# Kernel tuning notes

Measured on AMD Instinct MI355X. Metric: run time of the kernel, lower is better.

Reference implementation:

```python
import jax, jax.numpy as jnp
import numpy as np

B, C, H, W = 8, 256, 48, 48
CR = C // 8  # query/key channel dim of the 1x1 conv projections


def setup_inputs() -> dict:
    key = jax.random.key(0)
    ks = jax.random.split(key, 8)
    s = 0.05  # weight scale
    return {
        "feat_map": jax.random.normal(ks[0], (B, C, H, W), dtype=jnp.float32),
        "w1": jax.random.normal(ks[1], (CR, C), dtype=jnp.float32) * s,
        "b1": jax.random.normal(ks[2], (CR,), dtype=jnp.float32) * s,
        "w2": jax.random.normal(ks[3], (CR, C), dtype=jnp.float32) * s,
        "b2": jax.random.normal(ks[4], (CR,), dtype=jnp.float32) * s,
        "w3": jax.random.normal(ks[5], (C, C), dtype=jnp.float32) * s,
        "b3": jax.random.normal(ks[6], (C,), dtype=jnp.float32) * s,
        "gamma": jnp.asarray(0.1, dtype=jnp.float32),  # torch inits to 0; nonzero for a meaningful baseline
    }


def reference(feat_map, w1, b1, w2, b2, w3, b3, gamma):
    b, c, h, w = feat_map.shape
    n = h * w
    x = feat_map.reshape(b, c, n)                     # [B,C,N]
    # 1x1 convs == per-pixel channel matmuls
    q = jnp.einsum('dc,bcn->bnd', w1, x) + b1         # [B,N,C/8]
    k = jnp.einsum('dc,bcn->bdn', w2, x) + b2[None, :, None]  # [B,C/8,N]
    attn = jax.nn.softmax(jnp.einsum('bnd,bdm->bnm', q, k), axis=-1)  # [B,N,N]
    v = jnp.einsum('dc,bcn->bdn', w3, x) + b3[None, :, None]  # [B,C,N]
    # out[b,c,i] = sum_j v[b,c,j] * attn[b,i,j]  (matches bmm(v, attn^T))
    refine = jnp.einsum('bcj,bij->bci', v, attn).reshape(b, c, h, w)
    return gamma * refine + feat_map
```

## Files before the change

kernel.cpp:

```cpp
#include <hip/hip_runtime.h>
#include <stdint.h>

#define NB  8
#define NC  256
#define NCR 32
#define NSP 2304
#define LOG2E 1.44269504088896340736f

typedef __attribute__((ext_vector_type(8))) short short8;
typedef __attribute__((ext_vector_type(4))) float f32x4;
typedef __attribute__((ext_vector_type(4))) unsigned short us4;
typedef __attribute__((ext_vector_type(2))) unsigned int u32x2;

__device__ __forceinline__ unsigned short f2bf(float f) {
  union { float f; unsigned u; } a; a.f = f;
  unsigned r = (a.u + 0x7FFFu + ((a.u >> 16) & 1u)) >> 16;
  return (unsigned short)r;
}

__device__ __forceinline__ float fexp2(float x) {
#if __has_builtin(__builtin_amdgcn_exp2f)
  return __builtin_amdgcn_exp2f(x);
#else
  return __exp2f(x);
#endif
}

__device__ __forceinline__ u32x2 pack4bf(float a, float b, float c, float d) {
  u32x2 r;
#if __has_builtin(__builtin_amdgcn_cvt_pk_bf16_f32)
  typedef __attribute__((ext_vector_type(2))) __bf16 bf2;
  union { bf2 v; unsigned u; } lo, hi;
  lo.v = __builtin_amdgcn_cvt_pk_bf16_f32(a, b);
  hi.v = __builtin_amdgcn_cvt_pk_bf16_f32(c, d);
  r[0] = lo.u; r[1] = hi.u;
#else
  r[0] = (unsigned)f2bf(a) | ((unsigned)f2bf(b) << 16);
  r[1] = (unsigned)f2bf(c) | ((unsigned)f2bf(d) << 16);
#endif
  return r;
}

typedef __attribute__((address_space(1))) const void* gvoidp;
typedef __attribute__((address_space(3))) void* lvoidp;
#define GLOADLDS16(g, l) __builtin_amdgcn_global_load_lds((gvoidp)(g), (lvoidp)(l), 16, 0, 0)

__global__ __launch_bounds__(256) void k_proj(const float* __restrict__ x,
    const float* __restrict__ w1, const float* __restrict__ b1,
    const float* __restrict__ w2, const float* __restrict__ b2,
    const float* __restrict__ w3, const float* __restrict__ b3,
    unsigned short* __restrict__ Q, unsigned short* __restrict__ K,
    unsigned short* __restrict__ V) {
  __shared__ unsigned short xs[32][264];
  const int n0 = blockIdx.x * 32, b = blockIdx.y;
  const int t = threadIdx.x, lane = t & 63, wave = t >> 6;
  const int col = lane & 15, quad = lane >> 4;
  const float* xb = x + (size_t)b * NC * NSP;
#pragma unroll
  for (int p = 0; p < 8; ++p) {
    const int crow = (t >> 3) + p * 32;
    const int n4 = (t & 7) * 4;
    float4 v = *(const float4*)(xb + (size_t)crow * NSP + n0 + n4);
    xs[n4 + 0][crow] = f2bf(v.x);
    xs[n4 + 1][crow] = f2bf(v.y);
    xs[n4 + 2][crow] = f2bf(v.z);
    xs[n4 + 3][crow] = f2bf(v.w);
  }
  __syncthreads();
  const f32x4 zero4 = {0.f, 0.f, 0.f, 0.f};
  f32x4 acc[5][2];
#pragma unroll
  for (int i = 0; i < 5; ++i)
#pragma unroll
    for (int j = 0; j < 2; ++j) acc[i][j] = zero4;

  for (int kc = 0; kc < 8; ++kc) {
    short8 bf[2];
#pragma unroll
    for (int nt = 0; nt < 2; ++nt)
      bf[nt] = *(const short8*)&xs[nt * 16 + col][kc * 32 + quad * 8];
#pragma unroll
    for (int ml = 0; ml < 5; ++ml) {
      const int m0 = (wave * 5 + ml) * 16;
      const float* wbase; int roff;
      if (m0 < 32)      { wbase = w1; roff = m0; }
      else if (m0 < 64) { wbase = w2; roff = m0 - 32; }
      else              { wbase = w3; roff = m0 - 64; }
      const float* wp = wbase + (size_t)(roff + col) * NC + kc * 32 + quad * 8;
      float4 f0 = *(const float4*)wp;
      float4 f1 = *(const float4*)(wp + 4);
      short8 af;
      af[0] = f2bf(f0.x); af[1] = f2bf(f0.y); af[2] = f2bf(f0.z); af[3] = f2bf(f0.w);
      af[4] = f2bf(f1.x); af[5] = f2bf(f1.y); af[6] = f2bf(f1.z); af[7] = f2bf(f1.w);
#pragma unroll
      for (int nt = 0; nt < 2; ++nt)
        acc[ml][nt] = __builtin_amdgcn_mfma_f32_16x16x32_bf16(af, bf[nt], acc[ml][nt], 0, 0, 0);
    }
  }
#pragma unroll
  for (int ml = 0; ml < 5; ++ml) {
    const int m0 = (wave * 5 + ml) * 16;
    const float* bias;
    if (m0 < 32)      bias = b1 + m0;
    else if (m0 < 64) bias = b2 + (m0 - 32);
    else              bias = b3 + (m0 - 64);
    float bv[4];
#pragma unroll
    for (int r = 0; r < 4; ++r) bv[r] = bias[quad * 4 + r];
    if (m0 < 64) {
      unsigned short* dst = (m0 < 32) ? Q : K;
      const float scl = (m0 < 32) ? LOG2E : 1.0f;
      const int d0 = (m0 & 31) + quad * 4;
#pragma unroll
      for (int nt = 0; nt < 2; ++nt) {
        const int n = n0 + nt * 16 + col;
        us4 pk;
#pragma unroll
        for (int r = 0; r < 4; ++r) pk[r] = f2bf((acc[ml][nt][r] + bv[r]) * scl);
        *(us4*)(dst + ((size_t)b * NSP + n) * NCR + d0) = pk;
      }
    } else {
      const int cbase = m0 - 64 + quad * 4;
#pragma unroll
      for (int nt = 0; nt < 2; ++nt) {
        const int n = n0 + nt * 16 + col;
#pragma unroll
        for (int r = 0; r < 4; ++r)
          V[((size_t)b * NC + cbase + r) * NSP + n] = f2bf(acc[ml][nt][r] + bv[r]);
      }
    }
  }
}

__global__ __launch_bounds__(192) void k_attn(const unsigned short* __restrict__ Q,
    const unsigned short* __restrict__ K, const unsigned short* __restrict__ V,
    const float* __restrict__ feat, const float* __restrict__ gamma,
    float* __restrict__ out) {
  __shared__ __align__(16) unsigned short smem[23296];
  unsigned short* Vs = smem;
  unsigned short* Ps = smem + 16384;
  const int i0 = blockIdx.x * 48, ch = blockIdx.y * 128, b = blockIdx.z;
  const int t = threadIdx.x, lane = t & 63, wave = t >> 6;
  const int col = lane & 15, quad = lane >> 4;
  const int iw = i0 + wave * 16;
  const unsigned short* Qb = Q + (size_t)b * NSP * NCR;
  const unsigned short* Kb = K + (size_t)b * NSP * NCR;
  const unsigned short* Vb = V + (size_t)b * NC * NSP;
  unsigned short* PsW = Ps + wave * 2304;

  const short8 qa = *(const short8*)(Qb + (size_t)(iw + col) * NCR + quad * 8);
  const f32x4 zero4 = {0.f, 0.f, 0.f, 0.f};
  f32x4 acc[8];
#pragma unroll
  for (int ct = 0; ct < 8; ++ct) acc[ct] = zero4;
  float rs = 0.f;
  const int r8 = lane >> 3, pc = lane & 7, jcs = pc ^ r8;

  short8 kb[4];
#pragma unroll
  for (int mt = 0; mt < 4; ++mt)
    kb[mt] = *(const short8*)(Kb + (size_t)(mt * 16 + col) * NCR + quad * 8);
#pragma unroll
  for (int cix = 0; cix < 6; ++cix) {
    const int q = wave * 6 + cix;
    if (q < 16) {
      const unsigned short* g = Vb + (size_t)(ch + q * 8 + r8) * NSP + jcs * 8;
      GLOADLDS16(g, Vs + q * 512);
    }
  }
#pragma unroll
  for (int mt = 0; mt < 4; ++mt) {
    f32x4 s = __builtin_amdgcn_mfma_f32_16x16x32_bf16(kb[mt], qa, zero4, 0, 0, 0);
    const float e0 = fexp2(s[0]), e1 = fexp2(s[1]), e2 = fexp2(s[2]), e3 = fexp2(s[3]);
    rs += (e0 + e1) + (e2 + e3);
    *(u32x2*)(PsW + col * 72 + mt * 16 + quad * 4) = pack4bf(e0, e1, e2, e3);
  }

  for (int kc = 0; kc < 36; ++kc) {
    __syncthreads();
    const int bufc = kc & 1, bufn = bufc ^ 1;
    const int j1 = (kc + 1) * 64;
    const bool more = (kc + 1 < 36);
    if (more) {
#pragma unroll
      for (int mt = 0; mt < 4; ++mt)
        kb[mt] = *(const short8*)(Kb + (size_t)(j1 + mt * 16 + col) * NCR + quad * 8);
#pragma unroll
      for (int cix = 0; cix < 6; ++cix) {
        const int q = wave * 6 + cix;
        if (q < 16) {
          const unsigned short* g = Vb + (size_t)(ch + q * 8 + r8) * NSP + j1 + jcs * 8;
          GLOADLDS16(g, Vs + bufn * 8192 + q * 512);
        }
      }
    }
    const unsigned short* pwc = PsW + bufc * 1152;
    const unsigned short* vsc = Vs + bufc * 8192;
#pragma unroll
    for (int kk = 0; kk < 2; ++kk) {
      const short8 pa = *(const short8*)(pwc + col * 72 + kk * 32 + quad * 8);
#pragma unroll
      for (int ct = 0; ct < 8; ++ct) {
        const short8 vbf = *(const short8*)(vsc + (ct * 16 + col) * 64 +
                                            (((kk * 4 + quad) ^ (col & 7)) * 8));
        acc[ct] = __builtin_amdgcn_mfma_f32_16x16x32_bf16(pa, vbf, acc[ct], 0, 0, 0);
      }
    }
    if (more) {
      unsigned short* pwn = PsW + bufn * 1152;
#pragma unroll
      for (int mt = 0; mt < 4; ++mt) {
        f32x4 s = __builtin_amdgcn_mfma_f32_16x16x32_bf16(kb[mt], qa, zero4, 0, 0, 0);
        const float e0 = fexp2(s[0]), e1 = fexp2(s[1]), e2 = fexp2(s[2]), e3 = fexp2(s[3]);
        rs += (e0 + e1) + (e2 + e3);
        *(u32x2*)(pwn + col * 72 + mt * 16 + quad * 4) = pack4bf(e0, e1, e2, e3);
      }
    }
  }

  rs += __shfl_xor(rs, 16, 64);
  rs += __shfl_xor(rs, 32, 64);
  const float g = gamma[0];
  float rinv[4];
#pragma unroll
  for (int r = 0; r < 4; ++r) rinv[r] = g / __shfl(rs, quad * 4 + r, 64);

  const float* fb = feat + (size_t)b * NC * NSP;
  float* ob = out + (size_t)b * NC * NSP;
#pragma unroll
  for (int ct = 0; ct < 8; ++ct) {
    const size_t a0 = (size_t)(ch + ct * 16 + col) * NSP + iw + quad * 4;
    float4 f = *(const float4*)(fb + a0);
    float4 o;
    o.x = acc[ct][0] * rinv[0] + f.x;
    o.y = acc[ct][1] * rinv[1] + f.y;
    o.z = acc[ct][2] * rinv[2] + f.z;
    o.w = acc[ct][3] * rinv[3] + f.w;
    *(float4*)(ob + a0) = o;
  }
}

#define OFF_Q  0UL
#define OFF_K  1179648UL
#define OFF_V  2359296UL

extern "C" void kernel_launch(void* const* d_in, const int* in_sizes, int n_in,
                              void* d_out, int out_size, void* d_ws, size_t ws_size,
                              hipStream_t stream) {
  const float* feat  = (const float*)d_in[0];
  const float* w1    = (const float*)d_in[1];
  const float* b1    = (const float*)d_in[2];
  const float* w2    = (const float*)d_in[3];
  const float* b2    = (const float*)d_in[4];
  const float* w3    = (const float*)d_in[5];
  const float* b3    = (const float*)d_in[6];
  const float* gamma = (const float*)d_in[7];
  float* out = (float*)d_out;
  char* ws = (char*)d_ws;
  unsigned short* Q = (unsigned short*)(ws + OFF_Q);
  unsigned short* K = (unsigned short*)(ws + OFF_K);
  unsigned short* V = (unsigned short*)(ws + OFF_V);

  hipLaunchKernelGGL(k_proj, dim3(72, NB), dim3(256), 0, stream,
                     feat, w1, b1, w2, b2, w3, b3, Q, K, V);
  hipLaunchKernelGGL(k_attn, dim3(48, 2, NB), dim3(192), 0, stream,
                     Q, K, V, feat, gamma, out);
}
```

Before: 167.7 us.

## Split attention key dimension in two halves and combine partials in separate kernel

The attention kernel now splits the key/value sequence into two halves across blockIdx.y, doubling the grid from 768 to 1536 blocks. Each block uses 32-wide key chunks and a smaller LDS footprint, then writes unnormalized fp32 partial outputs and row sums to workspace. A new combine kernel adds the two partials, normalizes by the summed row sums, applies gamma and adds the residual. This trades extra global traffic and a third launch (about 37MB written and read back) for more parallelism and occupancy. It also drops the running softmax max, relying on scores staying small as the original did.

```diff
diff --git a/kernel.cpp b/kernel.cpp
--- a/kernel.cpp
+++ b/kernel.cpp
@@ -134,19 +134,20 @@
 
 __global__ __launch_bounds__(192) void k_attn(const unsigned short* __restrict__ Q,
     const unsigned short* __restrict__ K, const unsigned short* __restrict__ V,
-    const float* __restrict__ feat, const float* __restrict__ gamma,
-    float* __restrict__ out) {
-  __shared__ __align__(16) unsigned short smem[23296];
+    float* __restrict__ Op, float* __restrict__ lp) {
+  __shared__ __align__(16) unsigned short smem[12032];
   unsigned short* Vs = smem;
-  unsigned short* Ps = smem + 16384;
-  const int i0 = blockIdx.x * 48, ch = blockIdx.y * 128, b = blockIdx.z;
+  unsigned short* Ps = smem + 8192;
+  const int i0 = blockIdx.x * 48, b = blockIdx.z;
+  const int ch = (blockIdx.y & 1) * 128, jh = blockIdx.y >> 1;
+  const int jb = jh * 1152;
   const int t = threadIdx.x, lane = t & 63, wave = t >> 6;
   const int col = lane & 15, quad = lane >> 4;
   const int iw = i0 + wave * 16;
   const unsigned short* Qb = Q + (size_t)b * NSP * NCR;
   const unsigned short* Kb = K + (size_t)b * NSP * NCR;
   const unsigned short* Vb = V + (size_t)b * NC * NSP;
-  unsigned short* PsW = Ps + wave * 2304;
+  unsigned short* PsW = Ps + wave * 1280;
 
   const short8 qa = *(const short8*)(Qb + (size_t)(iw + col) * NCR + quad * 8);
   const f32x4 zero4 = {0.f, 0.f, 0.f, 0.f};
@@ -154,95 +155,106 @@
 #pragma unroll
   for (int ct = 0; ct < 8; ++ct) acc[ct] = zero4;
   float rs = 0.f;
-  const int r8 = lane >> 3, pc = lane & 7, jcs = pc ^ r8;
-
-  short8 kb[4];
-#pragma unroll
-  for (int mt = 0; mt < 4; ++mt)
-    kb[mt] = *(const short8*)(Kb + (size_t)(mt * 16 + col) * NCR + quad * 8);
-#pragma unroll
-  for (int cix = 0; cix < 6; ++cix) {
-    const int q = wave * 6 + cix;
-    if (q < 16) {
-      const unsigned short* g = Vb + (size_t)(ch + q * 8 + r8) * NSP + jcs * 8;
+  const int r4 = lane >> 2, pc = lane & 3, jcs = pc ^ (r4 & 3);
+
+  short8 kb[2];
+#pragma unroll
+  for (int mt = 0; mt < 2; ++mt)
+    kb[mt] = *(const short8*)(Kb + (size_t)(jb + mt * 16 + col) * NCR + quad * 8);
+#pragma unroll
+  for (int cix = 0; cix < 3; ++cix) {
+    const int q = wave * 3 + cix;
+    if (q < 8) {
+      const unsigned short* g = Vb + (size_t)(ch + q * 16 + r4) * NSP + jb + jcs * 8;
       GLOADLDS16(g, Vs + q * 512);
     }
   }
 #pragma unroll
-  for (int mt = 0; mt < 4; ++mt) {
+  for (int mt = 0; mt < 2; ++mt) {
     f32x4 s = __builtin_amdgcn_mfma_f32_16x16x32_bf16(kb[mt], qa, zero4, 0, 0, 0);
     const float e0 = fexp2(s[0]), e1 = fexp2(s[1]), e2 = fexp2(s[2]), e3 = fexp2(s[3]);
     rs += (e0 + e1) + (e2 + e3);
-    *(u32x2*)(PsW + col * 72 + mt * 16 + quad * 4) = pack4bf(e0, e1, e2, e3);
+    *(u32x2*)(PsW + col * 40 + mt * 16 + quad * 4) = pack4bf(e0, e1, e2, e3);
   }
 
   for (int kc = 0; kc < 36; ++kc) {
     __syncthreads();
     const int bufc = kc & 1, bufn = bufc ^ 1;
-    const int j1 = (kc + 1) * 64;
+    const int j1 = jb + (kc + 1) * 32;
     const bool more = (kc + 1 < 36);
     if (more) {
 #pragma unroll
-      for (int mt = 0; mt < 4; ++mt)
+      for (int mt = 0; mt < 2; ++mt)
         kb[mt] = *(const short8*)(Kb + (size_t)(j1 + mt * 16 + col) * NCR + quad * 8);
 #pragma unroll
-      for (int cix = 0; cix < 6; ++cix) {
-        const int q = wave * 6 + cix;
-        if (q < 16) {
-          const unsigned short* g = Vb + (size_t)(ch + q * 8 + r8) * NSP + j1 + jcs * 8;
-          GLOADLDS16(g, Vs + bufn * 8192 + q * 512);
+      for (int cix = 0; cix < 3; ++cix) {
+        const int q = wave * 3 + cix;
+        if (q < 8) {
+          const unsigned short* g = Vb + (size_t)(ch + q * 16 + r4) * NSP + j1 + jcs * 8;
+          GLOADLDS16(g, Vs + bufn * 4096 + q * 512);
         }
       }
     }
-    const unsigned short* pwc = PsW + bufc * 1152;
-    const unsigned short* vsc = Vs + bufc * 8192;
-#pragma unroll
-    for (int kk = 0; kk < 2; ++kk) {
-      const short8 pa = *(const short8*)(pwc + col * 72 + kk * 32 + quad * 8);
-#pragma unroll
-      for (int ct = 0; ct < 8; ++ct) {
-        const short8 vbf = *(const short8*)(vsc + (ct * 16 + col) * 64 +
-                                            (((kk * 4 + quad) ^ (col & 7)) * 8));
-        acc[ct] = __builtin_amdgcn_mfma_f32_16x16x32_bf16(pa, vbf, acc[ct], 0, 0, 0);
-      }
+    const unsigned short* pwc = PsW + bufc * 640;
+    const unsigned short* vsc = Vs + bufc * 4096;
+    const short8 pa = *(const short8*)(pwc + col * 40 + quad * 8);
+#pragma unroll
+    for (int ct = 0; ct < 8; ++ct) {
+      const short8 vbf = *(const short8*)(vsc + (ct * 16 + col) * 32 +
+                                          ((quad ^ (col & 3)) * 8));
+      acc[ct] = __builtin_amdgcn_mfma_f32_16x16x32_bf16(pa, vbf, acc[ct], 0, 0, 0);
     }
     if (more) {
-      unsigned short* pwn = PsW + bufn * 1152;
-#pragma unroll
-      for (int mt = 0; mt < 4; ++mt) {
+      unsigned short* pwn = PsW + bufn * 640;
+#pragma unroll
+      for (int mt = 0; mt < 2; ++mt) {
         f32x4 s = __builtin_amdgcn_mfma_f32_16x16x32_bf16(kb[mt], qa, zero4, 0, 0, 0);
         const float e0 = fexp2(s[0]), e1 = fexp2(s[1]), e2 = fexp2(s[2]), e3 = fexp2(s[3]);
         rs += (e0 + e1) + (e2 + e3);
-        *(u32x2*)(pwn + col * 72 + mt * 16 + quad * 4) = pack4bf(e0, e1, e2, e3);
+        *(u32x2*)(pwn + col * 40 + mt * 16 + quad * 4) = pack4bf(e0, e1, e2, e3);
       }
     }
   }
 
   rs += __shfl_xor(rs, 16, 64);
   rs += __shfl_xor(rs, 32, 64);
+  if (((blockIdx.y & 1) == 0) && quad == 0)
+    lp[((size_t)jh * NB + b) * NSP + iw + col] = rs;
+
+  float* Ob = Op + (((size_t)jh * NB + b) * NC + ch) * NSP;
+#pragma unroll
+  for (int ct = 0; ct < 8; ++ct)
+    *(f32x4*)(Ob + (size_t)(ct * 16 + col) * NSP + iw + quad * 4) = acc[ct];
+}
+
+__global__ __launch_bounds__(256) void k_combine(const float* __restrict__ Op,
+    const float* __restrict__ lp, const float* __restrict__ feat,
+    const float* __restrict__ gamma, float* __restrict__ out) {
+  const int tid = blockIdx.x * 256 + threadIdx.x;
+  const int b = tid / (NC * NSP / 4);
+  const int rem = tid - b * (NC * NSP / 4);
+  const int c = rem / (NSP / 4);
+  const int i4 = (rem - c * (NSP / 4)) * 4;
+  const size_t a = ((size_t)b * NC + c) * NSP + i4;
+  const float4 o0 = *(const float4*)(Op + a);
+  const float4 o1 = *(const float4*)(Op + (size_t)NB * NC * NSP + a);
+  const float4 l0 = *(const float4*)(lp + (size_t)b * NSP + i4);
+  const float4 l1 = *(const float4*)(lp + (size_t)(NB + b) * NSP + i4);
+  const float4 ft = *(const float4*)(feat + a);
   const float g = gamma[0];
-  float rinv[4];
-#pragma unroll
-  for (int r = 0; r < 4; ++r) rinv[r] = g / __shfl(rs, quad * 4 + r, 64);
-
-  const float* fb = feat + (size_t)b * NC * NSP;
-  float* ob = out + (size_t)b * NC * NSP;
-#pragma unroll
-  for (int ct = 0; ct < 8; ++ct) {
-    const size_t a0 = (size_t)(ch + ct * 16 + col) * NSP + iw + quad * 4;
-    float4 f = *(const float4*)(fb + a0);
-    float4 o;
-    o.x = acc[ct][0] * rinv[0] + f.x;
-    o.y = acc[ct][1] * rinv[1] + f.y;
-    o.z = acc[ct][2] * rinv[2] + f.z;
-    o.w = acc[ct][3] * rinv[3] + f.w;
-    *(float4*)(ob + a0) = o;
-  }
+  float4 o;
+  o.x = (o0.x + o1.x) * (g / (l0.x + l1.x)) + ft.x;
+  o.y = (o0.y + o1.y) * (g / (l0.y + l1.y)) + ft.y;
+  o.z = (o0.z + o1.z) * (g / (l0.z + l1.z)) + ft.z;
+  o.w = (o0.w + o1.w) * (g / (l0.w + l1.w)) + ft.w;
+  *(float4*)(out + a) = o;
 }
 
 #define OFF_Q  0UL
 #define OFF_K  1179648UL
 #define OFF_V  2359296UL
+#define OFF_OP 11796480UL
+#define OFF_LP 49545216UL
 
 extern "C" void kernel_launch(void* const* d_in, const int* in_sizes, int n_in,
                               void* d_out, int out_size, void* d_ws, size_t ws_size,
@@ -260,9 +272,13 @@
   unsigned short* Q = (unsigned short*)(ws + OFF_Q);
   unsigned short* K = (unsigned short*)(ws + OFF_K);
   unsigned short* V = (unsigned short*)(ws + OFF_V);
+  float* Op = (float*)(ws + OFF_OP);
+  float* lp = (float*)(ws + OFF_LP);
 
   hipLaunchKernelGGL(k_proj, dim3(72, NB), dim3(256), 0, stream,
                      feat, w1, b1, w2, b2, w3, b3, Q, K, V);
-  hipLaunchKernelGGL(k_attn, dim3(48, 2, NB), dim3(192), 0, stream,
-                     Q, K, V, feat, gamma, out);
-}
+  hipLaunchKernelGGL(k_attn, dim3(48, 4, NB), dim3(192), 0, stream,
+                     Q, K, V, Op, lp);
+  hipLaunchKernelGGL(k_combine, dim3(4608), dim3(256), 0, stream,
+                     Op, lp, feat, gamma, out);
+}
```

After: 175.6 us. +4.7%, slower.
